# Kernel optimization log

Measured on AMD Instinct MI355X. Metric: run time of the kernel, lower is better.

## Reference

```python
import jax, jax.numpy as jnp
import numpy as np

N = 65536          # nodes
E = 1048576        # edges
IN_C = 128
HID_C = 32
HEADS = 4
OUT_C = 64
NEG_SLOPE = 0.2
EPS = 1e-16


def gat_conv(x, edge_index, W, att_src, att_dst, bias, heads, out_c, concat):
    """PyG-style GATConv. x: [N, F_in]; edge_index: [2, E] (row=src, col=dst).
    W: [F_in, heads*out_c]; att_src/att_dst: [heads, out_c]; bias: [heads*out_c] or [out_c]."""
    src, dst = edge_index[0], edge_index[1]
    n = x.shape[0]
    h = (x @ W).reshape(n, heads, out_c)                      # [N, H, C]
    a_src = jnp.einsum('nhc,hc->nh', h, att_src)              # [N, H]
    a_dst = jnp.einsum('nhc,hc->nh', h, att_dst)              # [N, H]
    alpha = a_src[src] + a_dst[dst]                           # [E, H]
    alpha = jax.nn.leaky_relu(alpha, NEG_SLOPE)
    # segment softmax over incoming edges of each destination node
    amax = jax.ops.segment_max(alpha, dst, num_segments=n)    # [N, H]
    alpha = jnp.exp(alpha - amax[dst])
    denom = jax.ops.segment_sum(alpha, dst, num_segments=n)   # [N, H]
    alpha = alpha / (denom[dst] + EPS)
    # weighted scatter-add aggregation
    msgs = alpha[:, :, None] * h[src]                         # [E, H, C]
    out = jax.ops.segment_sum(msgs, dst, num_segments=n)      # [N, H, C]
    if concat:
        out = out.reshape(n, heads * out_c)
    else:
        out = out.mean(axis=1)
    return out + bias


def setup_inputs() -> dict:
    key = jax.random.key(0)
    ks = jax.random.split(key, 10)
    s_in = 1.0 / np.sqrt(IN_C)
    s_h = 1.0 / np.sqrt(HEADS * HID_C)
    x = jax.random.normal(ks[0], (N, IN_C), dtype=jnp.float32)
    edge_index = jax.random.randint(ks[1], (2, E), 0, N, dtype=jnp.int64)
    W1 = jax.random.normal(ks[2], (IN_C, HEADS * HID_C), dtype=jnp.float32) * s_in
    att_src1 = jax.random.normal(ks[3], (HEADS, HID_C), dtype=jnp.float32) * s_h
    att_dst1 = jax.random.normal(ks[4], (HEADS, HID_C), dtype=jnp.float32) * s_h
    b1 = jnp.zeros((HEADS * HID_C,), dtype=jnp.float32)
    W2 = jax.random.normal(ks[5], (HEADS * HID_C, OUT_C), dtype=jnp.float32) * s_h
    att_src2 = jax.random.normal(ks[6], (1, OUT_C), dtype=jnp.float32) * s_h
    att_dst2 = jax.random.normal(ks[7], (1, OUT_C), dtype=jnp.float32) * s_h
    b2 = jnp.zeros((OUT_C,), dtype=jnp.float32)
    return {"x": x, "edge_index": edge_index, "W1": W1, "att_src1": att_src1,
            "att_dst1": att_dst1, "b1": b1, "W2": W2, "att_src2": att_src2,
            "att_dst2": att_dst2, "b2": b2}


def reference(x, edge_index, W1, att_src1, att_dst1, b1, W2, att_src2, att_dst2, b2):
    # dropout is identity in eval mode
    h = gat_conv(x, edge_index, W1, att_src1, att_dst1, b1, HEADS, HID_C, concat=True)
    h = jax.nn.sigmoid(h)
    h = gat_conv(h, edge_index, W2, att_src2, att_dst2, b2, 1, OUT_C, concat=True)
    return jax.nn.sigmoid(h)
```

## Files before the change

### kernel.cpp

```cpp
#include <hip/hip_runtime.h>

#define N_NODES 65536
#define N_EDGES 1048576
#define NBUCK 256
#define PBLOCKS 256
#define EPB (N_EDGES / PBLOCKS)
#define K4CAP 6144
constexpr float NEG = 0.2f;
constexpr float EPS_ = 1e-16f;

typedef __attribute__((ext_vector_type(8))) short bf16x8;
typedef __attribute__((ext_vector_type(4))) float f32x4;

__device__ __forceinline__ unsigned short f2bf(float f) {
    unsigned int u = __float_as_uint(f);
    return (unsigned short)((u + 0x7fffu + ((u >> 16) & 1u)) >> 16);
}
__device__ __forceinline__ float bflo(unsigned int p) { return __uint_as_float(p << 16); }
__device__ __forceinline__ float bfhi(unsigned int p) { return __uint_as_float(p & 0xffff0000u); }
__device__ __forceinline__ float bf2f(unsigned short u) { return __uint_as_float((unsigned int)u << 16); }
__device__ __forceinline__ float lrelu_exp(float l) { return __expf(fmaxf(l, NEG * l)); }


__global__ __launch_bounds__(256) void coarse_hist(const int* __restrict__ ei,
                                                   int* __restrict__ hist_mat) {
    __shared__ int h[NBUCK];
    int t = threadIdx.x;
    h[t] = 0;
    __syncthreads();
    int base = blockIdx.x * EPB;
    #pragma unroll
    for (int i = 0; i < EPB / 256; ++i) {
        int d = ei[N_EDGES + base + i * 256 + t];
        atomicAdd(&h[d >> 8], 1);
    }
    __syncthreads();
    hist_mat[t * PBLOCKS + blockIdx.x] = h[t];
}

__global__ __launch_bounds__(1024) void scan_a(const int* __restrict__ in,
                                               int* __restrict__ out,
                                               int* __restrict__ bsum) {
    __shared__ int sm[1024];
    int t = threadIdx.x, i = blockIdx.x * 1024 + t;
    int v = in[i];
    sm[t] = v;
    __syncthreads();
    for (int off = 1; off < 1024; off <<= 1) {
        int u = (t >= off) ? sm[t - off] : 0;
        __syncthreads();
        sm[t] += u;
        __syncthreads();
    }
    out[i] = sm[t] - v;
    if (t == 1023) bsum[blockIdx.x] = sm[t];
}

__global__ __launch_bounds__(64) void scan_b(int* __restrict__ bsum,
                                             int* __restrict__ row_ptr) {
    int t = threadIdx.x;
    int v = bsum[t];
    int incl = v;
    #pragma unroll
    for (int off = 1; off < 64; off <<= 1) {
        int u = __shfl_up(incl, off);
        if (t >= off) incl += u;
    }
    bsum[t] = incl - v;
    if (t == 63) row_ptr[N_NODES] = incl;
}

__global__ __launch_bounds__(1024) void scan_c(int* __restrict__ arr,
                                               const int* __restrict__ bsum) {
    int i = blockIdx.x * 1024 + threadIdx.x;
    arr[i] += bsum[blockIdx.x];
}

__global__ __launch_bounds__(256) void partition_kernel(const int* __restrict__ ei,
                                                        const int* __restrict__ cursor_mat,
                                                        unsigned int* __restrict__ edge_part) {
    __shared__ int h[NBUCK];
    __shared__ int start[NBUCK];
    __shared__ int cur[NBUCK];
    __shared__ int gcur[NBUCK];
    __shared__ unsigned int stage[EPB];
    int t = threadIdx.x;
    h[t] = 0;
    gcur[t] = cursor_mat[t * PBLOCKS + blockIdx.x];
    __syncthreads();
    unsigned int ent[EPB / 256];
    int base = blockIdx.x * EPB;
    #pragma unroll
    for (int i = 0; i < EPB / 256; ++i) {
        int e = base + i * 256 + t;
        int s = ei[e], d = ei[N_EDGES + e];
        ent[i] = ((unsigned int)s << 16) | (unsigned int)d;
        atomicAdd(&h[d >> 8], 1);
    }
    __syncthreads();
    int v = h[t];
    start[t] = v;
    __syncthreads();
    for (int off = 1; off < 256; off <<= 1) {
        int u = (t >= off) ? start[t - off] : 0;
        __syncthreads();
        start[t] += u;
        __syncthreads();
    }
    int excl = start[t] - v;
    start[t] = excl;
    cur[t] = excl;
    __syncthreads();
    #pragma unroll
    for (int i = 0; i < EPB / 256; ++i) {
        int b = (int)((ent[i] & 0xffffu) >> 8);
        int slot = atomicAdd(&cur[b], 1);
        stage[slot] = ent[i];
    }
    __syncthreads();
    int s0 = t * (EPB / 256);
    #pragma unroll
    for (int i = 0; i < EPB / 256; ++i) {
        unsigned int p = stage[s0 + i];
        int b = (int)((p & 0xffffu) >> 8);
        edge_part[gcur[b] + (s0 + i - start[b])] = p;
    }
}

__global__ __launch_bounds__(256) void finalize_kernel(const unsigned int* __restrict__ edge_part,
                                                       const int* __restrict__ cursor_mat,
                                                       int* __restrict__ row_ptr,
                                                       int* __restrict__ csr_src) {
    __shared__ int h[256];
    __shared__ int sc[256];
    __shared__ int cur[256];
    __shared__ unsigned short stage[K4CAP];
    int t = threadIdx.x;
    int b = blockIdx.x;
    int cs = cursor_mat[b * PBLOCKS];
    int ce = (b == NBUCK - 1) ? N_EDGES : cursor_mat[(b + 1) * PBLOCKS];
    int cnt = ce - cs;
    h[t] = 0;
    __syncthreads();
    for (int i = t; i < cnt; i += 256)
        atomicAdd(&h[edge_part[cs + i] & 0xffu], 1);
    __syncthreads();
    int v = h[t];
    sc[t] = v;
    __syncthreads();
    for (int off = 1; off < 256; off <<= 1) {
        int u = (t >= off) ? sc[t - off] : 0;
        __syncthreads();
        sc[t] += u;
        __syncthreads();
    }
    int excl = sc[t] - v;
    row_ptr[b * 256 + t] = cs + excl;
    cur[t] = excl;
    __syncthreads();
    if (cnt <= K4CAP) {
        for (int i = t; i < cnt; i += 256) {
            unsigned int p = edge_part[cs + i];
            int slot = atomicAdd(&cur[p & 0xffu], 1);
            stage[slot] = (unsigned short)(p >> 16);
        }
        __syncthreads();
        for (int i = t; i < cnt; i += 256)
            csr_src[cs + i] = (int)stage[i];
    } else {
        for (int i = t; i < cnt; i += 256) {
            unsigned int p = edge_part[cs + i];
            int slot = atomicAdd(&cur[p & 0xffu], 1);
            csr_src[cs + slot] = (int)(p >> 16);
        }
    }
}


template <int OUTC>
__global__ __launch_bounds__(256) void gemm_mfma(const float* __restrict__ X,
                                                 const float* __restrict__ W,
                                                 unsigned short* __restrict__ H) {
    constexpr int NT = OUTC / 16;
    extern __shared__ unsigned short Wl[];
    int t = threadIdx.x;
    for (int idx = t; idx < OUTC * 128; idx += 256) {
        int j = idx & 7;
        int ln = (idx >> 3) & 63;
        int fc = idx >> 9;
        int kc = fc & 3, ct = fc >> 2;
        int k = kc * 32 + (ln >> 4) * 8 + j;
        int n = ct * 16 + (ln & 15);
        Wl[idx] = (unsigned short)f2bf(W[k * OUTC + n]);
    }
    __syncthreads();
    int wave = t >> 6, lane = t & 63;
    int m = lane & 15, quad = lane >> 4;
    int node_base = blockIdx.x * 64 + wave * 16;
    const float* xrow = X + (size_t)(node_base + m) * 128 + quad * 8;
    bf16x8 a[4];
    #pragma unroll
    for (int kc = 0; kc < 4; ++kc) {
        float4 u = *(const float4*)(xrow + kc * 32);
        float4 v = *(const float4*)(xrow + kc * 32 + 4);
        bf16x8 af;
        af[0] = (short)f2bf(u.x); af[1] = (short)f2bf(u.y);
        af[2] = (short)f2bf(u.z); af[3] = (short)f2bf(u.w);
        af[4] = (short)f2bf(v.x); af[5] = (short)f2bf(v.y);
        af[6] = (short)f2bf(v.z); af[7] = (short)f2bf(v.w);
        a[kc] = af;
    }
    #pragma unroll
    for (int ct = 0; ct < NT; ++ct) {
        f32x4 acc = {0.f, 0.f, 0.f, 0.f};
        #pragma unroll
        for (int kc = 0; kc < 4; ++kc) {
            bf16x8 bfr = *(const bf16x8*)(Wl + ((ct * 4 + kc) * 64 + lane) * 8);
            acc = __builtin_amdgcn_mfma_f32_16x16x32_bf16(a[kc], bfr, acc, 0, 0, 0);
        }
        #pragma unroll
        for (int r = 0; r < 4; ++r) {
            int row = quad * 4 + r;
            H[(size_t)(node_base + row) * OUTC + ct * 16 + m] = (unsigned short)f2bf(acc[r]);
        }
    }
}


__global__ __launch_bounds__(256) void att1_kernel(const unsigned int* __restrict__ h1u,
                                                   const float* __restrict__ as_w,
                                                   const float* __restrict__ ad_w,
                                                   float* __restrict__ a_src,
                                                   float* __restrict__ a_dst) {
    int wave = (blockIdx.x * 256 + threadIdx.x) >> 6;
    int lane = threadIdx.x & 63;
    unsigned int p = h1u[wave * 64 + lane];
    float h0 = bflo(p), h1v = bfhi(p);
    float2 sw = *(const float2*)(as_w + lane * 2);
    float2 dw = *(const float2*)(ad_w + lane * 2);
    float ps = h0 * sw.x + h1v * sw.y;
    float pd = h0 * dw.x + h1v * dw.y;
    #pragma unroll
    for (int m = 1; m < 16; m <<= 1) {
        ps += __shfl_xor(ps, m);
        pd += __shfl_xor(pd, m);
    }
    if ((lane & 15) == 0) {
        a_src[wave * 4 + (lane >> 4)] = ps;
        a_dst[wave * 4 + (lane >> 4)] = pd;
    }
}

__global__ __launch_bounds__(256) void att2_kernel(const unsigned short* __restrict__ h2u,
                                                   const float* __restrict__ as_w,
                                                   const float* __restrict__ ad_w,
                                                   float* __restrict__ a_src,
                                                   float* __restrict__ a_dst) {
    int wave = (blockIdx.x * 256 + threadIdx.x) >> 6;
    int lane = threadIdx.x & 63;
    float v = bf2f(h2u[wave * 64 + lane]);
    float ps = v * as_w[lane];
    float pd = v * ad_w[lane];
    #pragma unroll
    for (int m = 1; m < 64; m <<= 1) {
        ps += __shfl_xor(ps, m);
        pd += __shfl_xor(pd, m);
    }
    if (lane == 0) {
        a_src[wave] = ps;
        a_dst[wave] = pd;
    }
}


__global__ __launch_bounds__(256) void agg1_kernel(const int* __restrict__ row_ptr,
                                                   const int* __restrict__ csr_src,
                                                   const unsigned int* __restrict__ h1u,
                                                   const float* __restrict__ a_src,
                                                   const float* __restrict__ a_dst,
                                                   const float* __restrict__ b1,
                                                   float* __restrict__ x2) {
    int n = (blockIdx.x * 256 + threadIdx.x) >> 6;
    int lane = threadIdx.x & 63;
    int hd = lane >> 4;
    int j16 = lane & 15;
    int wbase = lane & 48;
    int c0 = lane * 2;
    float ad = a_dst[n * 4 + hd];
    int e = row_ptr[n], end = row_ptr[n + 1];
    float acc0 = 0.f, acc1 = 0.f, denom = 0.f;
    while (e + 16 <= end) {
        int s_l = csr_src[e + j16];
        float wv = lrelu_exp(a_src[s_l * 4 + hd] + ad);
        #pragma unroll
        for (int j = 0; j < 16; ++j) {
            int s = __shfl(s_l, j);
            float w = __shfl(wv, wbase + j);
            unsigned int p = h1u[(size_t)s * 64 + lane];
            denom += w;
            acc0 += w * bflo(p);
            acc1 += w * bfhi(p);
        }
        e += 16;
    }
    if (e < end) {
        int mb = end - e;
        int s_l = csr_src[e + (j16 < mb ? j16 : 0)];
        float wv = lrelu_exp(a_src[s_l * 4 + hd] + ad);
        #pragma unroll
        for (int j = 0; j < 16; ++j) {
            int s = __shfl(s_l, j);
            float w = (j < mb) ? __shfl(wv, wbase + j) : 0.f;
            unsigned int p = h1u[(size_t)s * 64 + lane];
            denom += w;
            acc0 += w * bflo(p);
            acc1 += w * bfhi(p);
        }
    }
    float inv = 1.f / (denom + EPS_);
    float o0 = acc0 * inv + b1[c0];
    float o1 = acc1 * inv + b1[c0 + 1];
    o0 = 1.f / (1.f + __expf(-o0));
    o1 = 1.f / (1.f + __expf(-o1));
    *(float2*)(x2 + (size_t)n * 128 + c0) = make_float2(o0, o1);
}

__global__ __launch_bounds__(256) void agg2_kernel(const int* __restrict__ row_ptr,
                                                   const int* __restrict__ csr_src,
                                                   const unsigned short* __restrict__ h2u,
                                                   const float* __restrict__ a_src,
                                                   const float* __restrict__ a_dst,
                                                   const float* __restrict__ b2,
                                                   float* __restrict__ out) {
    int n = (blockIdx.x * 256 + threadIdx.x) >> 6;
    int lane = threadIdx.x & 63;
    int j16 = lane & 15;
    float ad = a_dst[n];
    int e = row_ptr[n], end = row_ptr[n + 1];
    float acc = 0.f, denom = 0.f;
    while (e + 16 <= end) {
        int s_l = csr_src[e + j16];
        float wv = lrelu_exp(a_src[s_l] + ad);
        #pragma unroll
        for (int j = 0; j < 16; ++j) {
            int s = __shfl(s_l, j);
            float w = __shfl(wv, j);
            denom += w;
            acc += w * bf2f(h2u[(size_t)s * 64 + lane]);
        }
        e += 16;
    }
    if (e < end) {
        int mb = end - e;
        int s_l = csr_src[e + (j16 < mb ? j16 : 0)];
        float wv = lrelu_exp(a_src[s_l] + ad);
        #pragma unroll
        for (int j = 0; j < 16; ++j) {
            int s = __shfl(s_l, j);
            float w = (j < mb) ? __shfl(wv, j) : 0.f;
            denom += w;
            acc += w * bf2f(h2u[(size_t)s * 64 + lane]);
        }
    }
    float o = acc / (denom + EPS_) + b2[lane];
    out[(size_t)n * 64 + lane] = 1.f / (1.f + __expf(-o));
}


extern "C" void kernel_launch(void* const* d_in, const int* in_sizes, int n_in,
                              void* d_out, int out_size, void* d_ws, size_t ws_size,
                              hipStream_t stream) {
    (void)in_sizes; (void)n_in; (void)out_size; (void)ws_size;
    const float* x   = (const float*)d_in[0];
    const int*   ei  = (const int*)d_in[1];
    const float* W1  = (const float*)d_in[2];
    const float* as1 = (const float*)d_in[3];
    const float* ad1 = (const float*)d_in[4];
    const float* b1  = (const float*)d_in[5];
    const float* W2  = (const float*)d_in[6];
    const float* as2 = (const float*)d_in[7];
    const float* ad2 = (const float*)d_in[8];
    const float* b2  = (const float*)d_in[9];
    float* out = (float*)d_out;

    char* p = (char*)d_ws;
    auto alloc = [&](size_t bytes) -> void* {
        void* r = (void*)p;
        p += (bytes + 255) & ~(size_t)255;
        return r;
    };
    int* hist_mat   = (int*)alloc((size_t)NBUCK * PBLOCKS * 4);
    int* cursor_mat = (int*)alloc((size_t)NBUCK * PBLOCKS * 4);
    int* bsum       = (int*)alloc(64 * 4);
    unsigned int* edge_part = (unsigned int*)alloc((size_t)N_EDGES * 4);
    int* row_ptr    = (int*)alloc((size_t)(N_NODES + 1) * 4);
    int* csr_src    = (int*)alloc((size_t)N_EDGES * 4);
    unsigned short* h1 = (unsigned short*)alloc((size_t)N_NODES * 128 * 2);
    float* a_src1   = (float*)alloc((size_t)N_NODES * 4 * 4);
    float* a_dst1   = (float*)alloc((size_t)N_NODES * 4 * 4);
    float* x2       = (float*)alloc((size_t)N_NODES * 128 * 4);
    unsigned short* h2 = (unsigned short*)alloc((size_t)N_NODES * 64 * 2);
    float* a_src2   = (float*)alloc((size_t)N_NODES * 4);
    float* a_dst2   = (float*)alloc((size_t)N_NODES * 4);

    coarse_hist<<<PBLOCKS, 256, 0, stream>>>(ei, hist_mat);
    scan_a<<<64, 1024, 0, stream>>>(hist_mat, cursor_mat, bsum);
    scan_b<<<1, 64, 0, stream>>>(bsum, row_ptr);
    scan_c<<<64, 1024, 0, stream>>>(cursor_mat, bsum);
    partition_kernel<<<PBLOCKS, 256, 0, stream>>>(ei, cursor_mat, edge_part);
    finalize_kernel<<<NBUCK, 256, 0, stream>>>(edge_part, cursor_mat, row_ptr, csr_src);

    gemm_mfma<128><<<N_NODES / 64, 256, 128 * 128 * 2, stream>>>(x, W1, h1);
    att1_kernel<<<N_NODES / 4, 256, 0, stream>>>((const unsigned int*)h1, as1, ad1, a_src1, a_dst1);
    agg1_kernel<<<N_NODES / 4, 256, 0, stream>>>(row_ptr, csr_src, (const unsigned int*)h1,
                                                 a_src1, a_dst1, b1, x2);

    gemm_mfma<64><<<N_NODES / 64, 256, 128 * 64 * 2, stream>>>(x2, W2, h2);
    att2_kernel<<<N_NODES / 4, 256, 0, stream>>>(h2, as2, ad2, a_src2, a_dst2);
    agg2_kernel<<<N_NODES / 4, 256, 0, stream>>>(row_ptr, csr_src, h2, a_src2, a_dst2, b2, out);
}
```

Measured before the change: 274.2 us.

## Vectorize neighbor gathers in aggregation kernels and fold scan_b into scan_c

The aggregation kernels now gather 16-byte chunks per lane so several edges are processed in parallel across lane groups, then reduce the partial sums with cross-lane shuffles. The attention weight is packed as bf16 together with the 16-bit source index into one shuffled word. The single-block scan_b launch is merged into scan_c, which recomputes the block offsets in every block. The last row_ptr entry is set to a constant in finalize. This cuts gather instruction count and removes one launch, but adds shuffle reductions and rounds the attention weights to bf16.

```diff
diff --git a/kernel.cpp b/kernel.cpp
--- a/kernel.cpp
+++ b/kernel.cpp
@@ -56,24 +56,23 @@
     if (t == 1023) bsum[blockIdx.x] = sm[t];
 }
 
-__global__ __launch_bounds__(64) void scan_b(int* __restrict__ bsum,
-                                             int* __restrict__ row_ptr) {
-    int t = threadIdx.x;
-    int v = bsum[t];
-    int incl = v;
-    #pragma unroll
-    for (int off = 1; off < 64; off <<= 1) {
-        int u = __shfl_up(incl, off);
-        if (t >= off) incl += u;
-    }
-    bsum[t] = incl - v;
-    if (t == 63) row_ptr[N_NODES] = incl;
-}
-
 __global__ __launch_bounds__(1024) void scan_c(int* __restrict__ arr,
                                                const int* __restrict__ bsum) {
-    int i = blockIdx.x * 1024 + threadIdx.x;
-    arr[i] += bsum[blockIdx.x];
+    __shared__ int off[64];
+    int t = threadIdx.x;
+    if (t < 64) {
+        int v = bsum[t];
+        int incl = v;
+        #pragma unroll
+        for (int o = 1; o < 64; o <<= 1) {
+            int u = __shfl_up(incl, o);
+            if (t >= o) incl += u;
+        }
+        off[t] = incl - v;
+    }
+    __syncthreads();
+    int i = blockIdx.x * 1024 + t;
+    arr[i] += off[blockIdx.x];
 }
 
 __global__ __launch_bounds__(256) void partition_kernel(const int* __restrict__ ei,
@@ -137,6 +136,7 @@
     __shared__ unsigned short stage[K4CAP];
     int t = threadIdx.x;
     int b = blockIdx.x;
+    if (b == NBUCK - 1 && t == 0) row_ptr[N_NODES] = N_EDGES;
     int cs = cursor_mat[b * PBLOCKS];
     int ce = (b == NBUCK - 1) ? N_EDGES : cursor_mat[(b + 1) * PBLOCKS];
     int cnt = ce - cs;
@@ -282,88 +282,114 @@
                                                    float* __restrict__ x2) {
     int n = (blockIdx.x * 256 + threadIdx.x) >> 6;
     int lane = threadIdx.x & 63;
-    int hd = lane >> 4;
+    int quad = lane >> 4;
+    int col = lane & 15;
     int j16 = lane & 15;
-    int wbase = lane & 48;
-    int c0 = lane * 2;
-    float ad = a_dst[n * 4 + hd];
+    int hd_w = lane >> 4;
+    int hd_c = col >> 2;
+    float adw = a_dst[n * 4 + hd_w];
     int e = row_ptr[n], end = row_ptr[n + 1];
-    float acc0 = 0.f, acc1 = 0.f, denom = 0.f;
-    while (e + 16 <= end) {
-        int s_l = csr_src[e + j16];
-        float wv = lrelu_exp(a_src[s_l * 4 + hd] + ad);
-        #pragma unroll
-        for (int j = 0; j < 16; ++j) {
-            int s = __shfl(s_l, j);
-            float w = __shfl(wv, wbase + j);
-            unsigned int p = h1u[(size_t)s * 64 + lane];
+    float acc[8] = {};
+    float denom = 0.f;
+    while (e < end) {
+        int mb = end - e;
+        if (mb > 16) mb = 16;
+        int s_l = csr_src[e + (j16 < mb ? j16 : 0)];
+        float wv = lrelu_exp(a_src[s_l * 4 + hd_w] + adw);
+        unsigned int pack = ((unsigned int)f2bf(wv) << 16) | (unsigned int)s_l;
+        #pragma unroll
+        for (int g = 0; g < 4; ++g) {
+            int j = g * 4 + quad;
+            unsigned int pk = __shfl(pack, hd_c * 16 + j);
+            float w = (j < mb) ? __uint_as_float(pk & 0xffff0000u) : 0.f;
+            unsigned int s = pk & 0xffffu;
+            uint4 hv = *(const uint4*)(h1u + s * 64 + col * 4);
             denom += w;
-            acc0 += w * bflo(p);
-            acc1 += w * bfhi(p);
+            acc[0] += w * bflo(hv.x); acc[1] += w * bfhi(hv.x);
+            acc[2] += w * bflo(hv.y); acc[3] += w * bfhi(hv.y);
+            acc[4] += w * bflo(hv.z); acc[5] += w * bfhi(hv.z);
+            acc[6] += w * bflo(hv.w); acc[7] += w * bfhi(hv.w);
         }
         e += 16;
     }
-    if (e < end) {
-        int mb = end - e;
-        int s_l = csr_src[e + (j16 < mb ? j16 : 0)];
-        float wv = lrelu_exp(a_src[s_l * 4 + hd] + ad);
-        #pragma unroll
-        for (int j = 0; j < 16; ++j) {
-            int s = __shfl(s_l, j);
-            float w = (j < mb) ? __shfl(wv, wbase + j) : 0.f;
-            unsigned int p = h1u[(size_t)s * 64 + lane];
-            denom += w;
-            acc0 += w * bflo(p);
-            acc1 += w * bfhi(p);
-        }
-    }
-    float inv = 1.f / (denom + EPS_);
-    float o0 = acc0 * inv + b1[c0];
-    float o1 = acc1 * inv + b1[c0 + 1];
-    o0 = 1.f / (1.f + __expf(-o0));
-    o1 = 1.f / (1.f + __expf(-o1));
-    *(float2*)(x2 + (size_t)n * 128 + c0) = make_float2(o0, o1);
-}
+    #pragma unroll
+    for (int m = 16; m < 64; m <<= 1) {
+        denom += __shfl_xor(denom, m);
+        #pragma unroll
+        for (int i = 0; i < 8; ++i) acc[i] += __shfl_xor(acc[i], m);
+    }
+    if (quad == 0) {
+        float inv = 1.f / (denom + EPS_);
+        int c0 = col * 8;
+        float o[8];
+        #pragma unroll
+        for (int i = 0; i < 8; ++i) {
+            float v = acc[i] * inv + b1[c0 + i];
+            o[i] = 1.f / (1.f + __expf(-v));
+        }
+        float4* dst = (float4*)(x2 + (size_t)n * 128 + c0);
+        dst[0] = make_float4(o[0], o[1], o[2], o[3]);
+        dst[1] = make_float4(o[4], o[5], o[6], o[7]);
+    }
+}
+
 
 __global__ __launch_bounds__(256) void agg2_kernel(const int* __restrict__ row_ptr,
                                                    const int* __restrict__ csr_src,
-                                                   const unsigned short* __restrict__ h2u,
+                                                   const unsigned int* __restrict__ h2u,
                                                    const float* __restrict__ a_src,
                                                    const float* __restrict__ a_dst,
                                                    const float* __restrict__ b2,
                                                    float* __restrict__ out) {
     int n = (blockIdx.x * 256 + threadIdx.x) >> 6;
     int lane = threadIdx.x & 63;
+    int grp = lane >> 3;
+    int col = lane & 7;
     int j16 = lane & 15;
     float ad = a_dst[n];
     int e = row_ptr[n], end = row_ptr[n + 1];
-    float acc = 0.f, denom = 0.f;
-    while (e + 16 <= end) {
-        int s_l = csr_src[e + j16];
-        float wv = lrelu_exp(a_src[s_l] + ad);
-        #pragma unroll
-        for (int j = 0; j < 16; ++j) {
-            int s = __shfl(s_l, j);
-            float w = __shfl(wv, j);
-            denom += w;
-            acc += w * bf2f(h2u[(size_t)s * 64 + lane]);
-        }
-        e += 16;
-    }
-    if (e < end) {
+    float acc[8] = {};
+    float denom = 0.f;
+    while (e < end) {
         int mb = end - e;
+        if (mb > 16) mb = 16;
         int s_l = csr_src[e + (j16 < mb ? j16 : 0)];
         float wv = lrelu_exp(a_src[s_l] + ad);
-        #pragma unroll
-        for (int j = 0; j < 16; ++j) {
-            int s = __shfl(s_l, j);
-            float w = (j < mb) ? __shfl(wv, j) : 0.f;
+        unsigned int pack = ((unsigned int)f2bf(wv) << 16) | (unsigned int)s_l;
+        #pragma unroll
+        for (int g = 0; g < 2; ++g) {
+            int j = g * 8 + grp;
+            unsigned int pk = __shfl(pack, j);
+            float w = (j < mb) ? __uint_as_float(pk & 0xffff0000u) : 0.f;
+            unsigned int s = pk & 0xffffu;
+            uint4 hv = *(const uint4*)(h2u + s * 32 + col * 4);
             denom += w;
-            acc += w * bf2f(h2u[(size_t)s * 64 + lane]);
-        }
-    }
-    float o = acc / (denom + EPS_) + b2[lane];
-    out[(size_t)n * 64 + lane] = 1.f / (1.f + __expf(-o));
+            acc[0] += w * bflo(hv.x); acc[1] += w * bfhi(hv.x);
+            acc[2] += w * bflo(hv.y); acc[3] += w * bfhi(hv.y);
+            acc[4] += w * bflo(hv.z); acc[5] += w * bfhi(hv.z);
+            acc[6] += w * bflo(hv.w); acc[7] += w * bfhi(hv.w);
+        }
+        e += 16;
+    }
+    #pragma unroll
+    for (int m = 8; m < 64; m <<= 1) {
+        denom += __shfl_xor(denom, m);
+        #pragma unroll
+        for (int i = 0; i < 8; ++i) acc[i] += __shfl_xor(acc[i], m);
+    }
+    if (lane < 8) {
+        float inv = 1.f / (denom + EPS_);
+        int c0 = col * 8;
+        float o[8];
+        #pragma unroll
+        for (int i = 0; i < 8; ++i) {
+            float v = acc[i] * inv + b2[c0 + i];
+            o[i] = 1.f / (1.f + __expf(-v));
+        }
+        float4* dst = (float4*)(out + (size_t)n * 64 + c0);
+        dst[0] = make_float4(o[0], o[1], o[2], o[3]);
+        dst[1] = make_float4(o[4], o[5], o[6], o[7]);
+    }
 }
 
 
@@ -405,7 +431,6 @@
 
     coarse_hist<<<PBLOCKS, 256, 0, stream>>>(ei, hist_mat);
     scan_a<<<64, 1024, 0, stream>>>(hist_mat, cursor_mat, bsum);
-    scan_b<<<1, 64, 0, stream>>>(bsum, row_ptr);
     scan_c<<<64, 1024, 0, stream>>>(cursor_mat, bsum);
     partition_kernel<<<PBLOCKS, 256, 0, stream>>>(ei, cursor_mat, edge_part);
     finalize_kernel<<<NBUCK, 256, 0, stream>>>(edge_part, cursor_mat, row_ptr, csr_src);
@@ -417,5 +442,6 @@
 
     gemm_mfma<64><<<N_NODES / 64, 256, 128 * 64 * 2, stream>>>(x2, W2, h2);
     att2_kernel<<<N_NODES / 4, 256, 0, stream>>>(h2, as2, ad2, a_src2, a_dst2);
-    agg2_kernel<<<N_NODES / 4, 256, 0, stream>>>(row_ptr, csr_src, h2, a_src2, a_dst2, b2, out);
-}
+    agg2_kernel<<<N_NODES / 4, 256, 0, stream>>>(row_ptr, csr_src, (const unsigned int*)h2,
+                                                 a_src2, a_dst2, b2, out);
+}
```

New measurement: 262.8 us. 4.1% less time.
